# Performance work log

Measured on AMD Instinct MI355X. Metric: run time of the kernel, lower is better.

The kernel has to match this reference:

```python
import jax, jax.numpy as jnp
import numpy as np
import math

MODEL_DIM = 2048
NUM_Q_HEADS = 32
NUM_KV_HEADS = 8
HEAD_DIM = 64
ROPE_BASE = 10000.0
RMS_EPS = 1e-6


def setup_inputs() -> dict:
    key = jax.random.key(0)
    k1, k2, k3 = jax.random.split(key, 3)
    B, S = 2, 2048
    std = MODEL_DIM ** -0.5
    qkv_out = (NUM_Q_HEADS + 2 * NUM_KV_HEADS) * HEAD_DIM  # 3072
    return {
        "x": jax.random.normal(k1, (B, S, MODEL_DIM), dtype=jnp.float32),
        "w_qkv": jax.random.normal(k2, (qkv_out, MODEL_DIM), dtype=jnp.float32) * std,
        "w_out": jax.random.normal(k3, (MODEL_DIM, NUM_Q_HEADS * HEAD_DIM), dtype=jnp.float32) * std,
        "q_gamma": jnp.ones((HEAD_DIM,), dtype=jnp.float32),
        "k_gamma": jnp.ones((HEAD_DIM,), dtype=jnp.float32),
    }


def _rms_norm(x, gamma):
    # weight * sqrt(d) * F.normalize(x, dim=-1, eps): x / max(||x||_2, eps)
    norm = jnp.sqrt(jnp.sum(x * x, axis=-1, keepdims=True))
    scale = HEAD_DIM ** 0.5
    return (gamma * scale) * x / jnp.maximum(norm, RMS_EPS)


def _rope(x):
    # x: [B, H, S, hd]; rotate-half style RoPE, offset=0
    S = x.shape[2]
    half = HEAD_DIM // 2
    pos = jnp.arange(S, dtype=x.dtype)
    freqs = jnp.exp(-jnp.arange(half, dtype=x.dtype) * (math.log(ROPE_BASE) / half))
    theta = pos[:, None] * freqs[None, :]  # [S, half]
    sin, cos = jnp.sin(theta), jnp.cos(theta)
    x1, x2 = x[..., :half], x[..., half:]
    return jnp.concatenate([x1 * cos - x2 * sin, x1 * sin + x2 * cos], axis=-1)


def reference(x, w_qkv, w_out, q_gamma, k_gamma):
    B, S, D = x.shape
    groups = NUM_Q_HEADS // NUM_KV_HEADS
    qkv = jnp.einsum("bsd,ed->bse", x, w_qkv)  # [B,S,3072]
    qkv = qkv.reshape(B, S, NUM_Q_HEADS + 2 * NUM_KV_HEADS, HEAD_DIM).transpose(0, 2, 1, 3)
    q = qkv[:, :NUM_Q_HEADS]                                 # [B,Hq,S,hd]
    k = qkv[:, NUM_Q_HEADS:NUM_Q_HEADS + NUM_KV_HEADS]       # [B,Hk,S,hd]
    v = qkv[:, NUM_Q_HEADS + NUM_KV_HEADS:]                  # [B,Hk,S,hd]
    q = _rope(_rms_norm(q, q_gamma))
    k = _rope(_rms_norm(k, k_gamma))
    # GQA: repeat_interleave over head dim
    k = jnp.repeat(k, groups, axis=1)  # [B,Hq,S,hd]
    v = jnp.repeat(v, groups, axis=1)
    scale = 1.0 / (HEAD_DIM ** 0.5)
    scores = jnp.einsum("bhqd,bhkd->bhqk", q, k) * scale
    causal = jnp.tril(jnp.ones((S, S), dtype=bool))
    scores = jnp.where(causal, scores, jnp.finfo(scores.dtype).min)
    attn = jax.nn.softmax(scores, axis=-1)
    out = jnp.einsum("bhqk,bhkd->bhqd", attn, v)             # [B,Hq,S,hd]
    out = out.transpose(0, 2, 1, 3).reshape(B, S, NUM_Q_HEADS * HEAD_DIM)
    return jnp.einsum("bse,de->bsd", out, w_out)
```

## Files before the change

### kernel.cpp

```cpp
#include <hip/hip_runtime.h>
#include <hip/hip_bf16.h>
#include <stdint.h>

#define S_LEN  2048
#define BATCH  2
#define DMODEL 2048
#define EQKV   3072
#define HQ     32
#define HKV    8
#define HD     64
#define MROWS  (BATCH * S_LEN)

typedef unsigned short u16;
typedef __attribute__((ext_vector_type(8))) short bf16x8;
typedef __attribute__((ext_vector_type(4))) short bf16x4;
typedef __attribute__((ext_vector_type(4))) float f32x4;

__device__ __forceinline__ u16 f2bf(float f) {
  uint32_t x = __builtin_bit_cast(uint32_t, f);
  uint32_t r = x + 0x7fffu + ((x >> 16) & 1u);
  return (u16)(r >> 16);
}
__device__ __forceinline__ short f2bf_s(float f) {
  return __builtin_bit_cast(short, __float2bfloat16(f));
}
__device__ __forceinline__ float b2f(u16 u) {
  uint32_t x = ((uint32_t)u) << 16;
  return __builtin_bit_cast(float, x);
}
__device__ __forceinline__ float bflo(uint32_t u) {
  uint32_t x = u << 16; return __builtin_bit_cast(float, x);
}
__device__ __forceinline__ float bfhi(uint32_t u) {
  uint32_t x = u & 0xffff0000u; return __builtin_bit_cast(float, x);
}
__device__ __forceinline__ float fexp2(float x) {
#if __has_builtin(__builtin_amdgcn_exp2f)
  return __builtin_amdgcn_exp2f(x);
#else
  return exp2f(x);
#endif
}

__device__ __forceinline__ void gld16(const void* g, void* l) {
  __builtin_amdgcn_global_load_lds(
      (const __attribute__((address_space(1))) void*)g,
      (__attribute__((address_space(3))) void*)l, 16, 0, 0);
}

#define N8_X  ((size_t)MROWS * DMODEL / 8)
#define N8_WQ ((size_t)EQKV * DMODEL / 8)
#define N8_WO ((size_t)DMODEL * DMODEL / 8)
__global__ void cast3(const float* __restrict__ xa, const float* __restrict__ xb,
                      const float* __restrict__ xc,
                      u16* __restrict__ oa, u16* __restrict__ ob, u16* __restrict__ oc) {
  const int ntot = (int)(N8_X + N8_WQ + N8_WO);
  int stride = gridDim.x * blockDim.x;
  for (int i = blockIdx.x * blockDim.x + threadIdx.x; i < ntot; i += stride) {
    const float* in;
    u16* out;
    int j = i;
    if (j < (int)N8_X)                { in = xa; out = oa; }
    else if (j < (int)(N8_X + N8_WQ)) { in = xb; out = ob; j -= (int)N8_X; }
    else                              { in = xc; out = oc; j -= (int)(N8_X + N8_WQ); }
    const float4* p = (const float4*)(in + (size_t)j * 8);
    float4 a = p[0], b = p[1];
    uint32_t u0 = (uint32_t)f2bf(a.x) | ((uint32_t)f2bf(a.y) << 16);
    uint32_t u1 = (uint32_t)f2bf(a.z) | ((uint32_t)f2bf(a.w) << 16);
    uint32_t u2 = (uint32_t)f2bf(b.x) | ((uint32_t)f2bf(b.y) << 16);
    uint32_t u3 = (uint32_t)f2bf(b.z) | ((uint32_t)f2bf(b.w) << 16);
    *(uint4*)(out + (size_t)j * 8) = make_uint4(u0, u1, u2, u3);
  }
}

template<int OUT_BF16>
__global__ __launch_bounds__(512) void gemm_bt(const u16* __restrict__ A,
                                               const u16* __restrict__ Bm,
                                               void* __restrict__ Cv,
                                               int M, int N, int K, int nbx) {
  __shared__ u16 lA[128 * 64];
  __shared__ u16 lB[128 * 64];
  const int tid  = threadIdx.x;
  const int wave = tid >> 6;
  const int lane = tid & 63;

  const int nwg = gridDim.x;
  const int wg  = blockIdx.x;
  const int swz = (wg & 7) * (nwg >> 3) + (wg >> 3);
  const int brow = (swz % nbx) * 128;
  const int bcol = (swz / nbx) * 128;

  const int wr = (wave >> 2) * 64;
  const int wc = (wave & 3) * 32;
  const int fr = lane & 15;
  const int fq = lane >> 4;

  const int srow8 = lane >> 3;
  const int scol  = ((lane & 7) ^ srow8) * 8;

  f32x4 acc[4][2];
#pragma unroll
  for (int i = 0; i < 4; ++i)
#pragma unroll
    for (int j = 0; j < 2; ++j) acc[i][j] = (f32x4){0.f, 0.f, 0.f, 0.f};

  for (int k0 = 0; k0 < K; k0 += 64) {
    __syncthreads();
#pragma unroll
    for (int j = 0; j < 2; ++j) {
      int c = wave * 2 + j;
      int r = c * 8 + srow8;
      gld16(A  + (size_t)(brow + r) * K + k0 + scol, (char*)lA + c * 1024);
      gld16(Bm + (size_t)(bcol + r) * K + k0 + scol, (char*)lB + c * 1024);
    }
    __syncthreads();

    bf16x8 af[2][4], bfr[2][2];
#pragma unroll
    for (int kc = 0; kc < 2; ++kc) {
#pragma unroll
      for (int i = 0; i < 4; ++i) {
        int row = wr + i * 16 + fr;
        af[kc][i] = *(const bf16x8*)&lA[row * 64 + (((kc * 4 + fq) ^ (row & 7)) << 3)];
      }
#pragma unroll
      for (int j = 0; j < 2; ++j) {
        int row = wc + j * 16 + fr;
        bfr[kc][j] = *(const bf16x8*)&lB[row * 64 + (((kc * 4 + fq) ^ (row & 7)) << 3)];
      }
    }
#pragma unroll
    for (int kc = 0; kc < 2; ++kc)
#pragma unroll
      for (int i = 0; i < 4; ++i)
#pragma unroll
        for (int j = 0; j < 2; ++j)
          acc[i][j] = __builtin_amdgcn_mfma_f32_16x16x32_bf16(af[kc][i], bfr[kc][j], acc[i][j], 0, 0, 0);
  }

#pragma unroll
  for (int i = 0; i < 4; ++i)
#pragma unroll
    for (int j = 0; j < 2; ++j)
#pragma unroll
      for (int v = 0; v < 4; ++v) {
        int row = brow + wr + i * 16 + fq * 4 + v;
        int col = bcol + wc + j * 16 + fr;
        float val = acc[i][j][v];
        if (OUT_BF16) ((u16*)Cv)[(size_t)row * N + col] = f2bf(val);
        else          ((float*)Cv)[(size_t)row * N + col] = val;
      }
}

#define RMS_BLOCKS 40960
__global__ __launch_bounds__(256) void prep(const u16* __restrict__ qkv,
                                            u16* __restrict__ Qb,
                                            u16* __restrict__ Kb,
                                            u16* __restrict__ VTb,
                                            const float* __restrict__ qg,
                                            const float* __restrict__ kg) {
  __shared__ u16 T[64][68];
  if (blockIdx.x < RMS_BLOCKS) {
    int wid  = blockIdx.x * 4 + (threadIdx.x >> 6);
    int lane = threadIdx.x & 63;
    int head = wid % 40;
    int bs   = wid / 40;
    int s    = bs & (S_LEN - 1);
    int b    = bs >> 11;

    float v = b2f(qkv[(size_t)bs * EQKV + head * HD + lane]);
    float ss = v * v;
#pragma unroll
    for (int msk = 32; msk >= 1; msk >>= 1) ss += __shfl_xor(ss, msk);
    float norm = sqrtf(ss);
    float g = (head < 32) ? qg[lane] : kg[lane];
    float xv = v * (8.0f * g / fmaxf(norm, 1e-6f));
    float prt = __shfl_xor(xv, 32);
    int i = lane & 31;
    float freq  = expf(-(float)i * 0.28782313662425572f);
    float theta = (float)s * freq;
    float sn = sinf(theta), cs = cosf(theta);
    float res = (lane < 32) ? (xv * cs - prt * sn) : (prt * sn + xv * cs);
    u16 r = f2bf(res);
    if (head < 32) Qb[(((size_t)(b * HQ  + head     )) * S_LEN + s) * HD + lane] = r;
    else           Kb[(((size_t)(b * HKV + head - 32)) * S_LEN + s) * HD + lane] = r;
  } else {
    const int bid   = blockIdx.x - RMS_BLOCKS;
    const int stile = bid & 31;
    const int plane = bid >> 5;
    const int b = plane >> 3, kh = plane & 7;
    const int s0 = stile * 64;
    const int t = threadIdx.x;
    const int r = t >> 2, u0 = t & 3;

    const u16* src = qkv + ((size_t)(b * S_LEN + s0 + r)) * EQKV + (HQ + HKV + kh) * HD;
    *(uint4*)&T[r][u0 * 8]      = *(const uint4*)(src + u0 * 8);
    *(uint4*)&T[r][u0 * 8 + 32] = *(const uint4*)(src + u0 * 8 + 32);
    __syncthreads();

    const int d = t >> 2;
    u16* dst = VTb + ((size_t)plane * HD + d) * S_LEN + s0;
#pragma unroll
    for (int half = 0; half < 2; ++half) {
      int ub = u0 + half * 4;
      u16 tmp[8];
#pragma unroll
      for (int j = 0; j < 8; ++j) tmp[j] = T[ub * 8 + j][d];
      *(uint4*)(dst + ub * 8) = *(const uint4*)tmp;
    }
  }
}

__global__ __launch_bounds__(128) void attn_mfma(const u16* __restrict__ Qb,
                                                 const u16* __restrict__ Kb,
                                                 const u16* __restrict__ VTb,
                                                 u16* __restrict__ Ob) {
  __shared__ u16 Ks[64 * 64];
  __shared__ u16 Vt[64 * 64];
  const int tid  = threadIdx.x;
  const int wv   = tid >> 6;
  const int lane = tid & 63;
  const int fr   = lane & 15;
  const int fq   = lane >> 4;
  const int bh   = blockIdx.x;
  const int b    = bh >> 5, h = bh & 31, kh = h >> 2;
  const size_t kvbase = ((size_t)(b * HKV + kh)) * S_LEN * HD;

  const int tile   = 31 - (int)blockIdx.y;
  const int wqmin  = tile * 64 + wv * 32;
  const int kv_end = tile * 64 + 64;

  const int srow  = lane >> 3;
  const int sunit = (lane & 7) ^ srow;
  const u16* kp0 = Kb  + kvbase + (size_t)(wv * 32 + srow) * HD    + sunit * 8;
  const u16* vp0 = VTb + kvbase + (size_t)(wv * 32 + srow) * S_LEN + sunit * 8;

  const float QSCALE = 0.18033688011112042f;
  bf16x8 aq[2][2];
#pragma unroll
  for (int qf = 0; qf < 2; ++qf)
#pragma unroll
    for (int kc = 0; kc < 2; ++kc) {
      const u16* qp = Qb + ((size_t)bh * S_LEN + (wqmin + qf * 16 + fr)) * HD + kc * 32 + fq * 8;
      uint4 u = *(const uint4*)qp;
      uint32_t w[4] = {u.x, u.y, u.z, u.w};
      bf16x8 r;
#pragma unroll
      for (int i = 0; i < 4; ++i) {
        r[2 * i]     = f2bf_s(bflo(w[i]) * QSCALE);
        r[2 * i + 1] = f2bf_s(bfhi(w[i]) * QSCALE);
      }
      aq[qf][kc] = r;
    }

  const f32x4 Z4 = (f32x4){0.f, 0.f, 0.f, 0.f};
  bf16x4 ones;
#pragma unroll
  for (int v = 0; v < 4; ++v) ones[v] = (short)0x3F80;

  f32x4 o[2][4];
#pragma unroll
  for (int qf = 0; qf < 2; ++qf)
#pragma unroll
    for (int df = 0; df < 4; ++df) o[qf][df] = Z4;
  f32x4 lacc[2] = {Z4, Z4};

  for (int k0 = 0; k0 < kv_end; k0 += 64) {
    __syncthreads();
#pragma unroll
    for (int i = 0; i < 4; ++i)
      gld16(kp0 + (size_t)(k0 + i * 8) * HD, (char*)Ks + (wv * 4 + i) * 1024);
#pragma unroll
    for (int i = 0; i < 4; ++i)
      gld16(vp0 + k0 + (size_t)(i * 8) * S_LEN, (char*)Vt + (wv * 4 + i) * 1024);
    __syncthreads();

    f32x4 st[2][4];
    __builtin_amdgcn_s_setprio(1);
#pragma unroll
    for (int kf = 0; kf < 4; ++kf) {
      int row = kf * 16 + fr;
      bf16x8 ak0 = *(const bf16x8*)((char*)Ks + row * 128 +
                                    ((fq * 16) ^ ((row & 7) << 4)));
      bf16x8 ak1 = *(const bf16x8*)((char*)Ks + row * 128 +
                                    ((64 + fq * 16) ^ ((row & 7) << 4)));
#pragma unroll
      for (int qf = 0; qf < 2; ++qf) {
        f32x4 tt = __builtin_amdgcn_mfma_f32_16x16x32_bf16(ak0, aq[qf][0], Z4, 0, 0, 0);
        st[qf][kf] = __builtin_amdgcn_mfma_f32_16x16x32_bf16(ak1, aq[qf][1], tt, 0, 0, 0);
      }
    }
    __builtin_amdgcn_s_setprio(0);

    const bool need_mask = (k0 + 63 > wqmin);
    bf16x4 pb[2][4];
#pragma unroll
    for (int qf = 0; qf < 2; ++qf) {
      const int qrow = wqmin + qf * 16 + fr;
      if (need_mask) {
#pragma unroll
        for (int kf = 0; kf < 4; ++kf)
#pragma unroll
          for (int v = 0; v < 4; ++v) {
            int kvg = k0 + kf * 16 + fq * 4 + v;
            st[qf][kf][v] = (kvg > qrow) ? -1e30f : st[qf][kf][v];
          }
      }
#pragma unroll
      for (int kf = 0; kf < 4; ++kf) {
        bf16x4 pp;
#pragma unroll
        for (int v = 0; v < 4; ++v) pp[v] = f2bf_s(fexp2(st[qf][kf][v]));
        pb[qf][kf] = pp;
      }
    }

    __builtin_amdgcn_s_setprio(1);
#pragma unroll
    for (int df = 0; df < 4; ++df) {
      int row = df * 16 + fr;
#pragma unroll
      for (int kf = 0; kf < 4; ++kf) {
        bf16x4 av = *(const bf16x4*)((char*)Vt + row * 128 +
                                     ((kf * 32 + fq * 8) ^ ((row & 7) << 4)));
#pragma unroll
        for (int qf = 0; qf < 2; ++qf)
          o[qf][df] = __builtin_amdgcn_mfma_f32_16x16x16bf16_1k(av, pb[qf][kf], o[qf][df], 0, 0, 0);
      }
    }
#pragma unroll
    for (int kf = 0; kf < 4; ++kf)
#pragma unroll
      for (int qf = 0; qf < 2; ++qf)
        lacc[qf] = __builtin_amdgcn_mfma_f32_16x16x16bf16_1k(ones, pb[qf][kf], lacc[qf], 0, 0, 0);
    __builtin_amdgcn_s_setprio(0);
  }

#pragma unroll
  for (int qf = 0; qf < 2; ++qf) {
    float inv = 1.0f / lacc[qf][0];
    int grow = b * S_LEN + wqmin + qf * 16 + fr;
#pragma unroll
    for (int df = 0; df < 4; ++df) {
      u16* op = Ob + (size_t)grow * DMODEL + h * HD + df * 16 + fq * 4;
      uint32_t w0 = (uint32_t)f2bf(o[qf][df][0] * inv) | ((uint32_t)f2bf(o[qf][df][1] * inv) << 16);
      uint32_t w1 = (uint32_t)f2bf(o[qf][df][2] * inv) | ((uint32_t)f2bf(o[qf][df][3] * inv) << 16);
      *(uint2*)op = make_uint2(w0, w1);
    }
  }
}

extern "C" void kernel_launch(void* const* d_in, const int* in_sizes, int n_in,
                              void* d_out, int out_size, void* d_ws, size_t ws_size,
                              hipStream_t stream) {
  const float* x    = (const float*)d_in[0];
  const float* wqkv = (const float*)d_in[1];
  const float* wout = (const float*)d_in[2];
  const float* qg   = (const float*)d_in[3];
  const float* kg   = (const float*)d_in[4];
  float* out = (float*)d_out;
  char* ws = (char*)d_ws;

  const size_t MB = 1024 * 1024;
  u16* xb    = (u16*)(ws + 0 * MB);
  u16* wqkvb = (u16*)(ws + 16 * MB);
  u16* qkvb  = (u16*)(ws + 28 * MB);
  u16* Qb    = (u16*)(ws + 52 * MB);
  u16* Kb    = (u16*)(ws + 68 * MB);
  u16* VTb   = (u16*)(ws + 72 * MB);
  u16* Ob    = xb;
  u16* woutb = (u16*)(ws + 76 * MB);

  cast3<<<2048, 256, 0, stream>>>(x, wqkv, wout, xb, wqkvb, woutb);
  gemm_bt<1><<<(MROWS / 128) * (EQKV / 128), 512, 0, stream>>>(xb, wqkvb, qkvb, MROWS, EQKV, DMODEL, MROWS / 128);
  prep<<<RMS_BLOCKS + BATCH * HKV * 32, 256, 0, stream>>>(qkvb, Qb, Kb, VTb, qg, kg);
  attn_mfma<<<dim3(BATCH * HQ, 32), 128, 0, stream>>>(Qb, Kb, VTb, Ob);
  gemm_bt<0><<<(MROWS / 128) * (DMODEL / 128), 512, 0, stream>>>(Ob, woutb, out, MROWS, DMODEL, DMODEL, MROWS / 128);
}
```

Before: 213.4 us.

## Fuse RMSNorm, RoPE, and V transpose into the QKV GEMM epilogue

Removes the separate prep kernel and the intermediate bf16 qkv buffer. The QKV GEMM epilogue now stages its tile in shared memory and writes normalized, rotated Q/K (with the softmax scale folded into Q) and a transposed V directly. RoPE sin/cos values are precomputed once into a table inside the cast kernel, and attention no longer rescales Q on load. This saves a full round trip of qkv through global memory and one launch, at the cost of more shared memory and a heavier GEMM epilogue that uses only half the threads.

Result: slower. 226.0 us (+5.9%).

```diff
diff --git a/kernel.cpp b/kernel.cpp
--- a/kernel.cpp
+++ b/kernel.cpp
@@ -41,6 +41,12 @@
   return exp2f(x);
 #endif
 }
+__device__ __forceinline__ uint4 pk8(const u16* o) {
+  return make_uint4((uint32_t)o[0] | ((uint32_t)o[1] << 16),
+                    (uint32_t)o[2] | ((uint32_t)o[3] << 16),
+                    (uint32_t)o[4] | ((uint32_t)o[5] << 16),
+                    (uint32_t)o[6] | ((uint32_t)o[7] << 16));
+}
 
 __device__ __forceinline__ void gld16(const void* g, void* l) {
   __builtin_amdgcn_global_load_lds(
@@ -53,10 +59,18 @@
 #define N8_WO ((size_t)DMODEL * DMODEL / 8)
 __global__ void cast3(const float* __restrict__ xa, const float* __restrict__ xb,
                       const float* __restrict__ xc,
-                      u16* __restrict__ oa, u16* __restrict__ ob, u16* __restrict__ oc) {
+                      u16* __restrict__ oa, u16* __restrict__ ob, u16* __restrict__ oc,
+                      float2* __restrict__ tbl) {
   const int ntot = (int)(N8_X + N8_WQ + N8_WO);
+  int gid = blockIdx.x * blockDim.x + threadIdx.x;
+  if (gid < S_LEN * 32) {
+    int s = gid >> 5, i = gid & 31;
+    float freq  = __expf(-(float)i * 0.28782313662425572f);
+    float theta = (float)s * freq;
+    tbl[gid] = make_float2(sinf(theta), cosf(theta));
+  }
   int stride = gridDim.x * blockDim.x;
-  for (int i = blockIdx.x * blockDim.x + threadIdx.x; i < ntot; i += stride) {
+  for (int i = gid; i < ntot; i += stride) {
     const float* in;
     u16* out;
     int j = i;
@@ -73,13 +87,20 @@
   }
 }
 
-template<int OUT_BF16>
+template<int EPI>
 __global__ __launch_bounds__(512) void gemm_bt(const u16* __restrict__ A,
                                                const u16* __restrict__ Bm,
                                                void* __restrict__ Cv,
-                                               int M, int N, int K, int nbx) {
-  __shared__ u16 lA[128 * 64];
-  __shared__ u16 lB[128 * 64];
+                                               int M, int N, int K, int nbx,
+                                               u16* __restrict__ Qb,
+                                               u16* __restrict__ Kb,
+                                               u16* __restrict__ VTb,
+                                               const float* __restrict__ qg,
+                                               const float* __restrict__ kg,
+                                               const float2* __restrict__ tbl) {
+  __shared__ u16 sm[128 * 136];
+  u16* lA = sm;
+  u16* lB = sm + 8192;
   const int tid  = threadIdx.x;
   const int wave = tid >> 6;
   const int lane = tid & 63;
@@ -138,75 +159,78 @@
           acc[i][j] = __builtin_amdgcn_mfma_f32_16x16x32_bf16(af[kc][i], bfr[kc][j], acc[i][j], 0, 0, 0);
   }
 
-#pragma unroll
-  for (int i = 0; i < 4; ++i)
-#pragma unroll
-    for (int j = 0; j < 2; ++j)
-#pragma unroll
-      for (int v = 0; v < 4; ++v) {
-        int row = brow + wr + i * 16 + fq * 4 + v;
-        int col = bcol + wc + j * 16 + fr;
-        float val = acc[i][j][v];
-        if (OUT_BF16) ((u16*)Cv)[(size_t)row * N + col] = f2bf(val);
-        else          ((float*)Cv)[(size_t)row * N + col] = val;
-      }
-}
-
-#define RMS_BLOCKS 40960
-__global__ __launch_bounds__(256) void prep(const u16* __restrict__ qkv,
-                                            u16* __restrict__ Qb,
-                                            u16* __restrict__ Kb,
-                                            u16* __restrict__ VTb,
-                                            const float* __restrict__ qg,
-                                            const float* __restrict__ kg) {
-  __shared__ u16 T[64][68];
-  if (blockIdx.x < RMS_BLOCKS) {
-    int wid  = blockIdx.x * 4 + (threadIdx.x >> 6);
-    int lane = threadIdx.x & 63;
-    int head = wid % 40;
-    int bs   = wid / 40;
-    int s    = bs & (S_LEN - 1);
-    int b    = bs >> 11;
-
-    float v = b2f(qkv[(size_t)bs * EQKV + head * HD + lane]);
-    float ss = v * v;
-#pragma unroll
-    for (int msk = 32; msk >= 1; msk >>= 1) ss += __shfl_xor(ss, msk);
-    float norm = sqrtf(ss);
-    float g = (head < 32) ? qg[lane] : kg[lane];
-    float xv = v * (8.0f * g / fmaxf(norm, 1e-6f));
-    float prt = __shfl_xor(xv, 32);
-    int i = lane & 31;
-    float freq  = expf(-(float)i * 0.28782313662425572f);
-    float theta = (float)s * freq;
-    float sn = sinf(theta), cs = cosf(theta);
-    float res = (lane < 32) ? (xv * cs - prt * sn) : (prt * sn + xv * cs);
-    u16 r = f2bf(res);
-    if (head < 32) Qb[(((size_t)(b * HQ  + head     )) * S_LEN + s) * HD + lane] = r;
-    else           Kb[(((size_t)(b * HKV + head - 32)) * S_LEN + s) * HD + lane] = r;
+  if (EPI == 0) {
+#pragma unroll
+    for (int i = 0; i < 4; ++i)
+#pragma unroll
+      for (int j = 0; j < 2; ++j)
+#pragma unroll
+        for (int v = 0; v < 4; ++v) {
+          int row = brow + wr + i * 16 + fq * 4 + v;
+          int col = bcol + wc + j * 16 + fr;
+          ((float*)Cv)[(size_t)row * N + col] = acc[i][j][v];
+        }
   } else {
-    const int bid   = blockIdx.x - RMS_BLOCKS;
-    const int stile = bid & 31;
-    const int plane = bid >> 5;
-    const int b = plane >> 3, kh = plane & 7;
-    const int s0 = stile * 64;
-    const int t = threadIdx.x;
-    const int r = t >> 2, u0 = t & 3;
-
-    const u16* src = qkv + ((size_t)(b * S_LEN + s0 + r)) * EQKV + (HQ + HKV + kh) * HD;
-    *(uint4*)&T[r][u0 * 8]      = *(const uint4*)(src + u0 * 8);
-    *(uint4*)&T[r][u0 * 8 + 32] = *(const uint4*)(src + u0 * 8 + 32);
-    __syncthreads();
-
-    const int d = t >> 2;
-    u16* dst = VTb + ((size_t)plane * HD + d) * S_LEN + s0;
-#pragma unroll
-    for (int half = 0; half < 2; ++half) {
-      int ub = u0 + half * 4;
-      u16 tmp[8];
-#pragma unroll
-      for (int j = 0; j < 8; ++j) tmp[j] = T[ub * 8 + j][d];
-      *(uint4*)(dst + ub * 8) = *(const uint4*)tmp;
+    __syncthreads();
+    const int b = brow >> 11;
+    if (bcol >= 2560) {
+#pragma unroll
+      for (int i = 0; i < 4; ++i)
+#pragma unroll
+        for (int j = 0; j < 2; ++j) {
+          int e = bcol + wc + j * 16 + fr - 2560;
+          int s0 = (brow & 2047) + wr + i * 16 + fq * 4;
+          uint32_t w0 = (uint32_t)f2bf(acc[i][j][0]) | ((uint32_t)f2bf(acc[i][j][1]) << 16);
+          uint32_t w1 = (uint32_t)f2bf(acc[i][j][2]) | ((uint32_t)f2bf(acc[i][j][3]) << 16);
+          u16* dst = VTb + ((size_t)(b * HKV + (e >> 6)) * HD + (e & 63)) * S_LEN + s0;
+          *(uint2*)dst = make_uint2(w0, w1);
+        }
+    } else {
+#pragma unroll
+      for (int i = 0; i < 4; ++i)
+#pragma unroll
+        for (int j = 0; j < 2; ++j)
+#pragma unroll
+          for (int v = 0; v < 4; ++v)
+            sm[(wr + i * 16 + fq * 4 + v) * 136 + wc + j * 16 + fr] = f2bf(acc[i][j][v]);
+      __syncthreads();
+      if (tid < 256) {
+        const int lr = tid >> 1, h2 = tid & 1;
+        const int e0 = bcol + h2 * 64;
+        const bool isQ = (e0 < 2048);
+        const int head = isQ ? (e0 >> 6) : ((e0 - 2048) >> 6);
+        const int s    = (brow & 2047) + lr;
+        const float* gam = isQ ? qg : kg;
+        const u16* erow = sm + lr * 136 + h2 * 64;
+        float ss = 0.f;
+#pragma unroll
+        for (int c8 = 0; c8 < 8; ++c8) {
+          bf16x8 xv = *(const bf16x8*)(erow + c8 * 8);
+#pragma unroll
+          for (int j = 0; j < 8; ++j) { float f = b2f((u16)xv[j]); ss += f * f; }
+        }
+        float sb = 8.0f / fmaxf(sqrtf(ss), 1e-6f);
+        if (isQ) sb *= 0.18033688011112042f;
+        u16* dst = isQ ? Qb + (((size_t)(b * HQ  + head)) * S_LEN + s) * HD
+                       : Kb + (((size_t)(b * HKV + head)) * S_LEN + s) * HD;
+        const float2* trow = tbl + s * 32;
+#pragma unroll
+        for (int c0 = 0; c0 < 32; c0 += 8) {
+          bf16x8 x1 = *(const bf16x8*)(erow + c0);
+          bf16x8 x2 = *(const bf16x8*)(erow + 32 + c0);
+          u16 o1[8], o2[8];
+#pragma unroll
+          for (int j = 0; j < 8; ++j) {
+            float xv1 = b2f((u16)x1[j]) * gam[c0 + j]      * sb;
+            float xv2 = b2f((u16)x2[j]) * gam[32 + c0 + j] * sb;
+            float2 sc = trow[c0 + j];
+            o1[j] = f2bf(xv1 * sc.y - xv2 * sc.x);
+            o2[j] = f2bf(xv1 * sc.x + xv2 * sc.y);
+          }
+          *(uint4*)(dst + c0)      = pk8(o1);
+          *(uint4*)(dst + 32 + c0) = pk8(o2);
+        }
+      }
     }
   }
 }
@@ -235,23 +259,12 @@
   const u16* kp0 = Kb  + kvbase + (size_t)(wv * 32 + srow) * HD    + sunit * 8;
   const u16* vp0 = VTb + kvbase + (size_t)(wv * 32 + srow) * S_LEN + sunit * 8;
 
-  const float QSCALE = 0.18033688011112042f;
   bf16x8 aq[2][2];
 #pragma unroll
   for (int qf = 0; qf < 2; ++qf)
 #pragma unroll
-    for (int kc = 0; kc < 2; ++kc) {
-      const u16* qp = Qb + ((size_t)bh * S_LEN + (wqmin + qf * 16 + fr)) * HD + kc * 32 + fq * 8;
-      uint4 u = *(const uint4*)qp;
-      uint32_t w[4] = {u.x, u.y, u.z, u.w};
-      bf16x8 r;
-#pragma unroll
-      for (int i = 0; i < 4; ++i) {
-        r[2 * i]     = f2bf_s(bflo(w[i]) * QSCALE);
-        r[2 * i + 1] = f2bf_s(bfhi(w[i]) * QSCALE);
-      }
-      aq[qf][kc] = r;
-    }
+    for (int kc = 0; kc < 2; ++kc)
+      aq[qf][kc] = *(const bf16x8*)(Qb + ((size_t)bh * S_LEN + (wqmin + qf * 16 + fr)) * HD + kc * 32 + fq * 8);
 
   const f32x4 Z4 = (f32x4){0.f, 0.f, 0.f, 0.f};
   bf16x4 ones;
@@ -362,18 +375,19 @@
   char* ws = (char*)d_ws;
 
   const size_t MB = 1024 * 1024;
-  u16* xb    = (u16*)(ws + 0 * MB);
-  u16* wqkvb = (u16*)(ws + 16 * MB);
-  u16* qkvb  = (u16*)(ws + 28 * MB);
-  u16* Qb    = (u16*)(ws + 52 * MB);
-  u16* Kb    = (u16*)(ws + 68 * MB);
-  u16* VTb   = (u16*)(ws + 72 * MB);
-  u16* Ob    = xb;
-  u16* woutb = (u16*)(ws + 76 * MB);
-
-  cast3<<<2048, 256, 0, stream>>>(x, wqkv, wout, xb, wqkvb, woutb);
-  gemm_bt<1><<<(MROWS / 128) * (EQKV / 128), 512, 0, stream>>>(xb, wqkvb, qkvb, MROWS, EQKV, DMODEL, MROWS / 128);
-  prep<<<RMS_BLOCKS + BATCH * HKV * 32, 256, 0, stream>>>(qkvb, Qb, Kb, VTb, qg, kg);
+  u16*    xb    = (u16*)(ws + 0 * MB);
+  u16*    wqkvb = (u16*)(ws + 16 * MB);
+  float2* tbl   = (float2*)(ws + 28 * MB);
+  u16*    Qb    = (u16*)(ws + 52 * MB);
+  u16*    Kb    = (u16*)(ws + 68 * MB);
+  u16*    VTb   = (u16*)(ws + 72 * MB);
+  u16*    Ob    = xb;
+  u16*    woutb = (u16*)(ws + 76 * MB);
+
+  cast3<<<2048, 256, 0, stream>>>(x, wqkv, wout, xb, wqkvb, woutb, tbl);
+  gemm_bt<2><<<(MROWS / 128) * (EQKV / 128), 512, 0, stream>>>(
+      xb, wqkvb, nullptr, MROWS, EQKV, DMODEL, MROWS / 128, Qb, Kb, VTb, qg, kg, tbl);
   attn_mfma<<<dim3(BATCH * HQ, 32), 128, 0, stream>>>(Qb, Kb, VTb, Ob);
-  gemm_bt<0><<<(MROWS / 128) * (DMODEL / 128), 512, 0, stream>>>(Ob, woutb, out, MROWS, DMODEL, DMODEL, MROWS / 128);
-}
+  gemm_bt<0><<<(MROWS / 128) * (DMODEL / 128), 512, 0, stream>>>(
+      Ob, woutb, out, MROWS, DMODEL, DMODEL, MROWS / 128, nullptr, nullptr, nullptr, nullptr, nullptr, nullptr);
+}
```
